# Kernel tuning notes

Hardware: AMD Instinct MI355X
Metric: run time of the kernel (lower is better)

The kernel has to match this reference:

```python
import jax, jax.numpy as jnp
import numpy as np
import math

B, N, D = 4, 1024, 1024
H = 16
HD = D // H          # 64
TOP_K = 64
NUM_STATIC = 32


def setup_inputs() -> dict:
    key = jax.random.key(0)
    ks = jax.random.split(key, 10)
    s = 1.0 / math.sqrt(D)  # ~ nn.Linear default init scale
    inp = {
        "x": jax.random.normal(ks[0], (B, N, D), dtype=jnp.float32),
        "Wq": jax.random.uniform(ks[1], (D, D), jnp.float32, -s, s),
        "bq": jax.random.uniform(ks[2], (D,), jnp.float32, -s, s),
        "Wk": jax.random.uniform(ks[3], (D, D), jnp.float32, -s, s),
        "bk": jax.random.uniform(ks[4], (D,), jnp.float32, -s, s),
        "Wv": jax.random.uniform(ks[5], (D, D), jnp.float32, -s, s),
        "bv": jax.random.uniform(ks[6], (D,), jnp.float32, -s, s),
        "Wo": jax.random.uniform(ks[7], (D, D), jnp.float32, -s, s),
        "bo": jax.random.uniform(ks[8], (D,), jnp.float32, -s, s),
        "static_keys": jax.random.normal(ks[9], (NUM_STATIC, D), dtype=jnp.float32),
    }
    return inp


def _heads(t):
    # [B, N, D] -> [B, H, N, HD]
    return t.reshape(B, N, H, HD).transpose(0, 2, 1, 3)


def reference(x, Wq, bq, Wk, bk, Wv, bv, Wo, bo, static_keys):
    Q = _heads(x @ Wq.T + bq)
    K = _heads(x @ Wk.T + bk)
    V = _heads(x @ Wv.T + bv)

    # Replace the first NUM_STATIC key slots with learned static keys.
    K_stat = static_keys.reshape(1, NUM_STATIC, H, HD).transpose(0, 2, 1, 3)  # [1,H,S,HD]
    K_stat = jnp.broadcast_to(K_stat, (B, H, NUM_STATIC, HD))
    K = jnp.concatenate([K_stat, K[:, :, NUM_STATIC:, :]], axis=2)  # [B,H,N,HD]

    scores = jnp.einsum("bhnd,bhmd->bhnm", Q, K) / math.sqrt(HD)  # [B,H,N,N]

    # top-k mask: keep top_k scores per query, -inf elsewhere
    top_scores, top_idx = jax.lax.top_k(scores, TOP_K)  # [B,H,N,K]
    bi = jnp.arange(B)[:, None, None, None]
    hi = jnp.arange(H)[None, :, None, None]
    ni = jnp.arange(N)[None, None, :, None]
    masked = jnp.full(scores.shape, -jnp.inf, dtype=scores.dtype)
    masked = masked.at[bi, hi, ni, top_idx].set(top_scores)

    attn = jax.nn.softmax(masked, axis=-1)
    out = jnp.einsum("bhnm,bhmd->bhnd", attn, V)  # [B,H,N,HD]
    out = out.transpose(0, 2, 1, 3).reshape(B, N, D)
    return out @ Wo.T + bo
```

## Files before the change

kernel.cpp:

```cpp
#include <hip/hip_runtime.h>

#define NSTAT 32
#define MAXSEL 76

typedef __attribute__((ext_vector_type(8))) short bf16x8_t;
typedef __attribute__((ext_vector_type(4))) float f32x4_t;

#define GLOAD_LDS16(g, l) \
    __builtin_amdgcn_global_load_lds((const __attribute__((address_space(1))) void*)(g), \
                                     (__attribute__((address_space(3))) void*)(l), 16, 0, 0)

__device__ __forceinline__ ushort rtn_bf16(float a) {
    unsigned u = __float_as_uint(a);
    return (ushort)((u + 0x7FFFu + ((u >> 16) & 1u)) >> 16);
}
__device__ __forceinline__ void limb2(float a, ushort& h, ushort& l) {
    ushort hh = rtn_bf16(a);
    float fh = __uint_as_float(((unsigned)hh) << 16);
    float r1 = a - fh;
    l = rtn_bf16(r1);
    h = hh;
}

__global__ __launch_bounds__(256)
void decomp_w_kernel(const float* __restrict__ Wq, const float* __restrict__ Wk,
                     const float* __restrict__ Wv, const float* __restrict__ Wo,
                     ushort* __restrict__ WLq, ushort* __restrict__ WoLb)
{
    const int m = blockIdx.y;
    const float* src = (m == 0) ? Wq : (m == 1) ? Wk : (m == 2) ? Wv : Wo;
    const int idx = blockIdx.x * 256 + threadIdx.x;
    const int e8 = idx * 8;
    const int row = e8 >> 10, k0 = e8 & 1023;
    const int kt = k0 >> 5, q = (k0 >> 3) & 3;
    const size_t doff = ((size_t)row << 10) + (size_t)(kt * 32) + (size_t)((q ^ (row & 3)) * 8);

    float4 v0 = *(const float4*)(src + e8);
    float4 v1 = *(const float4*)(src + e8 + 4);
    float f[8] = {v0.x, v0.y, v0.z, v0.w, v1.x, v1.y, v1.z, v1.w};

    const size_t Mi = (size_t)1 << 20;
    ushort h[8], l[8];
    #pragma unroll
    for (int e = 0; e < 8; ++e) limb2(f[e], h[e], l[e]);
    ushort* H = (m == 3) ? WoLb : WLq + (size_t)(m * 2) * Mi;
    ushort* L = H + Mi;
    *(ushort4*)(H + doff)     = make_ushort4(h[0],h[1],h[2],h[3]);
    *(ushort4*)(H + doff + 4) = make_ushort4(h[4],h[5],h[6],h[7]);
    *(ushort4*)(L + doff)     = make_ushort4(l[0],l[1],l[2],l[3]);
    *(ushort4*)(L + doff + 4) = make_ushort4(l[4],l[5],l[6],l[7]);
}

__global__ __launch_bounds__(256, 3)
void limb_gemm_kernel(const float* __restrict__ A,
                      const ushort* __restrict__ WLq, const ushort* __restrict__ WoLb,
                      const float* __restrict__ bq, const float* __restrict__ bk,
                      const float* __restrict__ bv, const float* __restrict__ bo,
                      const float* __restrict__ statk,
                      float* __restrict__ Qw, float* __restrict__ Vw,
                      ushort* __restrict__ KHo, ushort* __restrict__ KLo,
                      float* __restrict__ Cout, int is_out)
{
    __shared__ __align__(16) ushort Al[2][128][32];
    __shared__ __align__(16) ushort Bl[2][2][128][32];

    const int t = threadIdx.x;
    const int bx = blockIdx.x, by = blockIdx.y;
    const int mode = is_out ? 3 : (int)blockIdx.z;
    const int wc0 = bx * 128;
    const int arow0 = by * 128;

    const size_t Mi = (size_t)1 << 20;
    const ushort* BpH;
    const float* bias;
    if (mode == 0)      { BpH = WLq;          bias = bq; }
    else if (mode == 1) { BpH = WLq + 2*Mi;   bias = bk; }
    else if (mode == 2) { BpH = WLq + 4*Mi;   bias = bv; }
    else                { BpH = WoLb;         bias = bo; }
    const ushort* BpL = BpH + Mi;

    const int ll = t & 63, w = t >> 6;

    f32x4_t acc[4][4];
    #pragma unroll
    for (int i = 0; i < 4; ++i)
        #pragma unroll
        for (int j = 0; j < 4; ++j) acc[i][j] = (f32x4_t){0.f, 0.f, 0.f, 0.f};

    auto stageB = [&](int kt, int bb) {
        #pragma unroll
        for (int limb = 0; limb < 2; ++limb) {
            const ushort* src = limb ? BpL : BpH;
            #pragma unroll
            for (int call = 0; call < 2; ++call) {
                int chunk = (w * 2 + call) * 64 + ll;
                int eoff = chunk * 8;
                int row = eoff >> 5, qp = (eoff >> 3) & 3;
                const ushort* g = src + ((size_t)(wc0 + row) << 10) + kt * 32 + qp * 8;
                char* l = ((char*)&Bl[bb][limb][0][0]) + (w * 2 + call) * 1024;
                GLOAD_LDS16(g, l);
            }
        }
    };
    const int srow = t >> 1, skh = (t & 1) * 16;
    auto loadA = [&](int kt, float4* a4) {
        const float* p = A + (((size_t)(arow0 + srow)) << 10) + kt * 32 + skh;
        a4[0] = *(const float4*)(p + 0);
        a4[1] = *(const float4*)(p + 4);
        a4[2] = *(const float4*)(p + 8);
        a4[3] = *(const float4*)(p + 12);
    };
    auto writeA = [&](const float4* a4) {
        float f[16];
        #pragma unroll
        for (int i = 0; i < 4; ++i) {
            f[i*4+0] = a4[i].x; f[i*4+1] = a4[i].y; f[i*4+2] = a4[i].z; f[i*4+3] = a4[i].w;
        }
        ushort h[16], lo[16];
        #pragma unroll
        for (int e = 0; e < 16; ++e) limb2(f[e], h[e], lo[e]);
        const int sw = srow & 3;
        #pragma unroll
        for (int qq = 0; qq < 2; ++qq) {
            int q = (skh >> 3) + qq;
            int qo = (q ^ sw) * 8;
            bf16x8_t vH, vL;
            #pragma unroll
            for (int e = 0; e < 8; ++e) {
                vH[e] = (short)h[qq*8+e]; vL[e] = (short)lo[qq*8+e];
            }
            *(bf16x8_t*)&Al[0][srow][qo] = vH;
            *(bf16x8_t*)&Al[1][srow][qo] = vL;
        }
    };

    const int wr = (w >> 1) * 64, wcv = (w & 1) * 64;
    const int fr = ll & 15, kg = ll >> 4;

    auto compute = [&](int bb) {
        bf16x8_t af[4][2];
        #pragma unroll
        for (int i = 0; i < 4; ++i) {
            int row = wr + i * 16 + fr;
            int qo = (kg ^ (row & 3)) * 8;
            af[i][0] = *(const bf16x8_t*)&Al[0][row][qo];
            af[i][1] = *(const bf16x8_t*)&Al[1][row][qo];
        }
        #pragma unroll
        for (int j = 0; j < 4; ++j) {
            int row = wcv + j * 16 + fr;
            int qo = (kg ^ (row & 3)) * 8;
            bf16x8_t b0 = *(const bf16x8_t*)&Bl[bb][0][row][qo];
            bf16x8_t b1 = *(const bf16x8_t*)&Bl[bb][1][row][qo];
            #pragma unroll
            for (int i = 0; i < 4; ++i) {
                acc[i][j] = __builtin_amdgcn_mfma_f32_16x16x32_bf16(af[i][0], b0, acc[i][j], 0, 0, 0);
                acc[i][j] = __builtin_amdgcn_mfma_f32_16x16x32_bf16(af[i][0], b1, acc[i][j], 0, 0, 0);
                acc[i][j] = __builtin_amdgcn_mfma_f32_16x16x32_bf16(af[i][1], b0, acc[i][j], 0, 0, 0);
            }
        }
    };

    float4 a4[4];
    loadA(0, a4);
    writeA(a4);
    stageB(0, 0);
    __syncthreads();

    float4 a4n[4];
    for (int kt = 0; kt < 32; ++kt) {
        int bb = kt & 1;
        if (kt < 31) {
            stageB(kt + 1, bb ^ 1);
            loadA(kt + 1, a4n);
        }
        compute(bb);
        __syncthreads();
        if (kt < 31) writeA(a4n);
        __syncthreads();
    }

    #pragma unroll
    for (int i = 0; i < 4; ++i) {
        #pragma unroll
        for (int j = 0; j < 4; ++j) {
            int c = wc0 + wcv + j * 16 + (ll & 15);
            float bv_ = bias[c];
            #pragma unroll
            for (int q = 0; q < 4; ++q) {
                int gr = arow0 + wr + i * 16 + (kg) * 4 + q;
                float v = acc[i][j][q] + bv_;
                if (mode == 3) {
                    Cout[(size_t)gr * 1024 + c] = v;
                } else {
                    int b = gr >> 10, n = gr & 1023;
                    int h = c >> 6, d = c & 63;
                    size_t bhn = ((size_t)(b * 16 + h)) * 1024 + n;
                    if (mode == 1) {
                        if (n < NSTAT) v = statk[n * 1024 + c];
                        ushort kh, klo;
                        limb2(v, kh, klo);
                        size_t off = bhn * 64 + (size_t)(((d >> 3) ^ (n & 7)) * 8) + (d & 7);
                        KHo[off] = kh;
                        KLo[off] = klo;
                    } else {
                        float* Out = (mode == 0) ? Qw : Vw;
                        Out[bhn * 64 + d] = v;
                    }
                }
            }
        }
    }
}

__device__ __forceinline__ void radix_stage7(int* __restrict__ hist, int r, int l,
                                             const unsigned* __restrict__ ku,
                                             unsigned pref, unsigned mask, int shift,
                                             int tgt, int2* __restrict__ piv)
{
    #pragma unroll
    for (int b = 0; b < 8; ++b) hist[(l*8 + b)*33 + r] = 0;
    __syncthreads();
    #pragma unroll
    for (int j = 0; j < 64; ++j) {
        unsigned k = ku[j];
        if ((k & mask) == pref)
            atomicAdd(&hist[(int)((k >> shift) & 127u)*33 + r], 1);
    }
    __syncthreads();
    int seg = 0;
    #pragma unroll
    for (int b = 0; b < 8; ++b) seg += hist[(l*8 + b)*33 + r];
    int suf = seg;
    #pragma unroll
    for (int off = 1; off < 16; off <<= 1) {
        int v = __shfl_down(suf, off, 16);
        suf += (l + off < 16) ? v : 0;
    }
    const int above = suf - seg;
    if (above < tgt && above + seg >= tgt) {
        int c = above;
        #pragma unroll
        for (int b = 7; b >= 0; --b) {
            int h = hist[(l*8 + b)*33 + r];
            if (c + h >= tgt) { piv[r] = make_int2(l*8 + b, tgt - c); break; }
            c += h;
        }
    }
    __syncthreads();
}

__global__ __launch_bounds__(512, 4)
void attn_mfma_kernel(const float* __restrict__ Qw,
                      const ushort* __restrict__ KH, const ushort* __restrict__ KL,
                      const float* __restrict__ Vw, float* __restrict__ outp)
{
    __shared__ __align__(16) char pool[58368];
    __shared__ int2 piv[32];
    __shared__ int defc[32], bndc[32];
    __shared__ float rs_def[32], rs_bnd[32], rowsum[32];

    ushort* Klds0 = (ushort*)pool;
    ushort* Klds1 = Klds0 + 8192;
    int* hist = (int*)pool;
    float (*Qs)[68]  = (float(*)[68])(pool + 32768);
    float (*sc)[132] = (float(*)[132])(pool + 41472);
    uint2 (*sel)[MAXSEL] = (uint2(*)[MAXSEL])(pool + 32768);

    const int t = threadIdx.x;
    const int bid0 = blockIdx.x;
    const int bid = (bid0 & 7) * 256 + (bid0 >> 3);
    const int qt = bid & 31;
    const int bh = bid >> 5;
    const int n0 = qt * 32;
    const float* Qbase = Qw + ((size_t)bh * 1024 + n0) * 64;
    const float* Vbase = Vw + (size_t)bh * 1024 * 64;
    const ushort* KHb = KH + (size_t)bh * 1024 * 64;
    const ushort* KLb = KL + (size_t)bh * 1024 * 64;

    const int ll = t & 63;
    const int w  = t >> 6;
    const int qh = w >> 2;
    const int kr = w & 3;
    const int r  = t >> 4, l = t & 15;

    {
        int q = t >> 4, dq = (t & 15) * 4;
        *(float4*)&Qs[q][dq] = *(const float4*)(Qbase + q * 64 + dq);
    }
    auto stageK = [&](int c) {
        const size_t cb = (size_t)c * 8192;
        #pragma unroll
        for (int i = 0; i < 2; ++i) {
            int boff = i * 8192 + w * 1024;
            GLOAD_LDS16(KHb + cb + boff / 2 + ll * 8, ((char*)Klds0) + boff);
            GLOAD_LDS16(KLb + cb + boff / 2 + ll * 8, ((char*)Klds1) + boff);
        }
    };
    stageK(0);
    __syncthreads();

    bf16x8_t aH[2], aL[2];
    {
        const int arow = qh * 16 + (ll & 15), akg = ll >> 4;
        #pragma unroll
        for (int s = 0; s < 2; ++s) {
            const float* qp = &Qs[arow][s*32 + akg*8];
            float4 q0 = *(const float4*)qp;
            float4 q1 = *(const float4*)(qp + 4);
            float qv[8] = {q0.x,q0.y,q0.z,q0.w,q1.x,q1.y,q1.z,q1.w};
            #pragma unroll
            for (int j = 0; j < 8; ++j) {
                ushort hh, lo2;
                limb2(qv[j], hh, lo2);
                aH[s][j] = (short)hh; aL[s][j] = (short)lo2;
            }
        }
    }
    __syncthreads();

    unsigned ku[64];
    unsigned kumax = 0u;

    #pragma unroll
    for (int c = 0; c < 8; ++c) {
        #pragma unroll
        for (int tile = 0; tile < 2; ++tile) {
            const int m0 = kr * 32 + tile * 16;
            const int brow = m0 + (ll & 15);
            f32x4_t a_ = {0.f, 0.f, 0.f, 0.f};
            #pragma unroll
            for (int s = 0; s < 2; ++s) {
                int q2 = (s*4 + (ll >> 4)) ^ (brow & 7);
                int off = brow*64 + q2*8;
                bf16x8_t bH = *(const bf16x8_t*)&Klds0[off];
                bf16x8_t bL = *(const bf16x8_t*)&Klds1[off];
                a_ = __builtin_amdgcn_mfma_f32_16x16x32_bf16(aH[s], bH, a_, 0, 0, 0);
                a_ = __builtin_amdgcn_mfma_f32_16x16x32_bf16(aH[s], bL, a_, 0, 0, 0);
                a_ = __builtin_amdgcn_mfma_f32_16x16x32_bf16(aL[s], bH, a_, 0, 0, 0);
            }
            const int qr = qh * 16 + (ll >> 4) * 4;
            const int mcol = m0 + (ll & 15);
            sc[qr+0][mcol] = a_[0];
            sc[qr+1][mcol] = a_[1];
            sc[qr+2][mcol] = a_[2];
            sc[qr+3][mcol] = a_[3];
        }
        __syncthreads();

        if (c < 7) stageK(c + 1);
        {
            float4 v0 = *(const float4*)&sc[r][l*8];
            float4 v1 = *(const float4*)&sc[r][l*8 + 4];
            float vv[8] = {v0.x,v0.y,v0.z,v0.w,v1.x,v1.y,v1.z,v1.w};
            #pragma unroll
            for (int e = 0; e < 8; ++e) {
                float vc = fminf(fmaxf(vv[e], -31.9f), 31.9f);
                unsigned q = (unsigned)(int)fmaf(vc, 32768.f, 1048576.f);
                ku[c*8 + e] = q;
                kumax = (q > kumax) ? q : kumax;
            }
        }
        __syncthreads();
    }

    #pragma unroll
    for (int off = 8; off; off >>= 1) {
        unsigned o = __shfl_xor(kumax, off, 16);
        kumax = (o > kumax) ? o : kumax;
    }

    if (t < 32) { defc[t] = 0; bndc[t] = 0; }

    int tgt = 64;
    radix_stage7(hist, r, l, ku, 0u, 0u, 14, tgt, piv);
    unsigned pref = (unsigned)piv[r].x << 14; tgt = piv[r].y;
    radix_stage7(hist, r, l, ku, pref, 0x1FC000u, 7, tgt, piv);
    pref |= (unsigned)piv[r].x << 7; tgt = piv[r].y;
    radix_stage7(hist, r, l, ku, pref, 0x1FFF80u, 0, tgt, piv);
    const unsigned thr = pref | (unsigned)piv[r].x;

    const unsigned bhi = thr + 2u;
    const unsigned blo = thr - 2u;
    float lsd = 0.f, lsb = 0.f;
    #pragma unroll
    for (int j = 0; j < 64; ++j) {
        unsigned k = ku[j];
        if (k > bhi) {
            float wgt = __expf((float)(int)(k - kumax) * 3.814697265625e-6f);
            int slot = atomicAdd(&defc[r], 1);
            sel[r][slot] = make_uint2((unsigned)((j >> 3)*128 + l*8 + (j & 7)), __float_as_uint(wgt));
            lsd += wgt;
        } else if (k >= blo) {
            int bp = atomicAdd(&bndc[r], 1);
            int slot = (MAXSEL - 1) - bp;
            if (slot >= 64) {
                float wgt = __expf((float)(int)(k - kumax) * 3.814697265625e-6f);
                sel[r][slot] = make_uint2((unsigned)((j >> 3)*128 + l*8 + (j & 7)), __float_as_uint(wgt));
                lsb += wgt;
            }
        }
    }
    #pragma unroll
    for (int off = 8; off; off >>= 1) {
        lsd += __shfl_xor(lsd, off, 16);
        lsb += __shfl_xor(lsb, off, 16);
    }
    if (l == 0) { rs_def[r] = lsd; rs_bnd[r] = lsb; }
    __syncthreads();

    if (t < 32) {
        int D = defc[t], m = bndc[t];
        float frac = (float)(64 - D) / (float)m;
        int mm = (m < MAXSEL - 64) ? m : (MAXSEL - 64);
        for (int i = 0; i < mm; ++i) {
            uint2 p = sel[t][(MAXSEL - 1) - i];
            p.y = __float_as_uint(__uint_as_float(p.y) * frac);
            sel[t][(MAXSEL - 1) - i] = p;
        }
        bndc[t] = mm;
        rowsum[t] = rs_def[t] + frac * rs_bnd[t];
    }
    __syncthreads();

    {
        const int pr = t >> 4;
        const int d4 = (t & 15) * 4;
        const int bb = bh >> 4, hh = bh & 15;
        const int D = defc[pr], m = bndc[pr];
        float4 a = make_float4(0.f, 0.f, 0.f, 0.f);
        for (int j = 0; j < D; ++j) {
            uint2 p = sel[pr][j];
            float wv = __uint_as_float(p.y);
            float4 v = *(const float4*)(Vbase + (size_t)p.x * 64 + d4);
            a.x += wv * v.x; a.y += wv * v.y; a.z += wv * v.z; a.w += wv * v.w;
        }
        for (int i = 0; i < m; ++i) {
            uint2 p = sel[pr][(MAXSEL - 1) - i];
            float wv = __uint_as_float(p.y);
            float4 v = *(const float4*)(Vbase + (size_t)p.x * 64 + d4);
            a.x += wv * v.x; a.y += wv * v.y; a.z += wv * v.z; a.w += wv * v.w;
        }
        float inv = 1.0f / rowsum[pr];
        a.x *= inv; a.y *= inv; a.z *= inv; a.w *= inv;
        *(float4*)(outp + ((size_t)bb * 1024 + (n0 + pr)) * 1024 + hh * 64 + d4) = a;
    }
}

extern "C" void kernel_launch(void* const* d_in, const int* in_sizes, int n_in,
                              void* d_out, int out_size, void* d_ws, size_t ws_size,
                              hipStream_t stream) {
    const float* x     = (const float*)d_in[0];
    const float* Wq    = (const float*)d_in[1];
    const float* bq    = (const float*)d_in[2];
    const float* Wk    = (const float*)d_in[3];
    const float* bk    = (const float*)d_in[4];
    const float* Wv    = (const float*)d_in[5];
    const float* bv    = (const float*)d_in[6];
    const float* Wo    = (const float*)d_in[7];
    const float* bo    = (const float*)d_in[8];
    const float* statk = (const float*)d_in[9];
    float* out = (float*)d_out;
    char* base = (char*)d_ws;

    const size_t MiB = (size_t)1 << 20;
    float*  Qw   = (float*)(base);
    float*  Vw   = (float*)(base + 16*MiB);
    ushort* KH   = (ushort*)(base + 32*MiB);
    ushort* KL   = (ushort*)(base + 40*MiB);
    ushort* WoLb = (ushort*)(base + 48*MiB);
    ushort* WLq  = (ushort*)(base + 52*MiB);
    float*  op   = (float*)(base + 52*MiB);

    dim3 gd(512, 4);
    decomp_w_kernel<<<gd, 256, 0, stream>>>(Wq, Wk, Wv, Wo, WLq, WoLb);

    dim3 g1(8, 32, 3);
    limb_gemm_kernel<<<g1, 256, 0, stream>>>(x, WLq, WoLb, bq, bk, bv, bo, statk,
                                             Qw, Vw, KH, KL, nullptr, 0);

    attn_mfma_kernel<<<2048, 512, 0, stream>>>(Qw, KH, KL, Vw, op);

    dim3 g2(8, 32, 1);
    limb_gemm_kernel<<<g2, 256, 0, stream>>>(op, WLq, WoLb, bq, bk, bv, bo, statk,
                                             Qw, Vw, KH, KL, out, 1);
}
```

Before: 302.5 us.

## Double-buffer K tiles with 16 smaller chunks and simplify top-k selection pass

The score loop now processes 16 chunks of 64 keys instead of 8 chunks of 128. K staging for the next chunk goes into a second LDS buffer before the current chunk's MFMA, and scores also alternate between two buffers, so one barrier per iteration is removed and the load overlaps compute. The selection pass collects every candidate at or above the lower bound in one atomic-append list. Exponentials are then computed relative to the threshold instead of a tracked maximum, which drops the max reduction and the serial single-thread boundary rescale. The V gather is unrolled by two to raise memory-level parallelism. Risks are larger LDS use (possibly lower occupancy), a loop that is no longer unrolled, and overflow of the exp if scores sit far above the threshold.

```diff
diff --git a/kernel.cpp b/kernel.cpp
--- a/kernel.cpp
+++ b/kernel.cpp
@@ -255,17 +255,14 @@
                       const ushort* __restrict__ KH, const ushort* __restrict__ KL,
                       const float* __restrict__ Vw, float* __restrict__ outp)
 {
-    __shared__ __align__(16) char pool[58368];
+    __shared__ __align__(16) char pool[59904];
     __shared__ int2 piv[32];
-    __shared__ int defc[32], bndc[32];
-    __shared__ float rs_def[32], rs_bnd[32], rowsum[32];
-
-    ushort* Klds0 = (ushort*)pool;
-    ushort* Klds1 = Klds0 + 8192;
+    __shared__ int cnt[32];
+    __shared__ float rowsum[32];
+
     int* hist = (int*)pool;
-    float (*Qs)[68]  = (float(*)[68])(pool + 32768);
-    float (*sc)[132] = (float(*)[132])(pool + 41472);
-    uint2 (*sel)[MAXSEL] = (uint2(*)[MAXSEL])(pool + 32768);
+    float (*Qs)[68] = (float(*)[68])(pool + 32768);
+    uint2 (*sel)[MAXSEL] = (uint2(*)[MAXSEL])pool;
 
     const int t = threadIdx.x;
     const int bid0 = blockIdx.x;
@@ -288,16 +285,16 @@
         int q = t >> 4, dq = (t & 15) * 4;
         *(float4*)&Qs[q][dq] = *(const float4*)(Qbase + q * 64 + dq);
     }
-    auto stageK = [&](int c) {
-        const size_t cb = (size_t)c * 8192;
-        #pragma unroll
-        for (int i = 0; i < 2; ++i) {
-            int boff = i * 8192 + w * 1024;
-            GLOAD_LDS16(KHb + cb + boff / 2 + ll * 8, ((char*)Klds0) + boff);
-            GLOAD_LDS16(KLb + cb + boff / 2 + ll * 8, ((char*)Klds1) + boff);
-        }
+    auto stageK = [&](int c, int kb) {
+        const ushort* gH = KHb + (size_t)c * 4096 + t * 8;
+        const ushort* gL = KLb + (size_t)c * 4096 + t * 8;
+        char* dH = pool + kb * 16384 + t * 16;
+        char* dL = pool + kb * 16384 + 8192 + t * 16;
+        GLOAD_LDS16(gH, dH);
+        GLOAD_LDS16(gL, dL);
     };
-    stageK(0);
+    stageK(0, 0);
+    if (t < 32) cnt[t] = 0;
     __syncthreads();
 
     bf16x8_t aH[2], aL[2];
@@ -317,60 +314,48 @@
             }
         }
     }
-    __syncthreads();
 
     unsigned ku[64];
-    unsigned kumax = 0u;
-
-    #pragma unroll
-    for (int c = 0; c < 8; ++c) {
-        #pragma unroll
-        for (int tile = 0; tile < 2; ++tile) {
-            const int m0 = kr * 32 + tile * 16;
-            const int brow = m0 + (ll & 15);
+
+    #pragma unroll 1
+    for (int c = 0; c < 16; ++c) {
+        const int kb = c & 1;
+        float (*scb)[72] = (float(*)[72])(pool + 41472 + kb * 9216);
+        if (c < 15) stageK(c + 1, kb ^ 1);
+
+        {
+            const ushort* KH_l = (const ushort*)(pool + kb * 16384);
+            const ushort* KL_l = KH_l + 4096;
+            const int brow = kr * 16 + (ll & 15);
             f32x4_t a_ = {0.f, 0.f, 0.f, 0.f};
             #pragma unroll
             for (int s = 0; s < 2; ++s) {
                 int q2 = (s*4 + (ll >> 4)) ^ (brow & 7);
                 int off = brow*64 + q2*8;
-                bf16x8_t bH = *(const bf16x8_t*)&Klds0[off];
-                bf16x8_t bL = *(const bf16x8_t*)&Klds1[off];
+                bf16x8_t bH = *(const bf16x8_t*)&KH_l[off];
+                bf16x8_t bL = *(const bf16x8_t*)&KL_l[off];
                 a_ = __builtin_amdgcn_mfma_f32_16x16x32_bf16(aH[s], bH, a_, 0, 0, 0);
                 a_ = __builtin_amdgcn_mfma_f32_16x16x32_bf16(aH[s], bL, a_, 0, 0, 0);
                 a_ = __builtin_amdgcn_mfma_f32_16x16x32_bf16(aL[s], bH, a_, 0, 0, 0);
             }
             const int qr = qh * 16 + (ll >> 4) * 4;
-            const int mcol = m0 + (ll & 15);
-            sc[qr+0][mcol] = a_[0];
-            sc[qr+1][mcol] = a_[1];
-            sc[qr+2][mcol] = a_[2];
-            sc[qr+3][mcol] = a_[3];
+            scb[qr+0][brow] = a_[0];
+            scb[qr+1][brow] = a_[1];
+            scb[qr+2][brow] = a_[2];
+            scb[qr+3][brow] = a_[3];
         }
         __syncthreads();
 
-        if (c < 7) stageK(c + 1);
         {
-            float4 v0 = *(const float4*)&sc[r][l*8];
-            float4 v1 = *(const float4*)&sc[r][l*8 + 4];
-            float vv[8] = {v0.x,v0.y,v0.z,v0.w,v1.x,v1.y,v1.z,v1.w};
-            #pragma unroll
-            for (int e = 0; e < 8; ++e) {
+            float4 v4 = *(const float4*)&scb[r][l*4];
+            float vv[4] = {v4.x, v4.y, v4.z, v4.w};
+            #pragma unroll
+            for (int e = 0; e < 4; ++e) {
                 float vc = fminf(fmaxf(vv[e], -31.9f), 31.9f);
-                unsigned q = (unsigned)(int)fmaf(vc, 32768.f, 1048576.f);
-                ku[c*8 + e] = q;
-                kumax = (q > kumax) ? q : kumax;
-            }
-        }
-        __syncthreads();
-    }
-
-    #pragma unroll
-    for (int off = 8; off; off >>= 1) {
-        unsigned o = __shfl_xor(kumax, off, 16);
-        kumax = (o > kumax) ? o : kumax;
-    }
-
-    if (t < 32) { defc[t] = 0; bndc[t] = 0; }
+                ku[c*4 + e] = (unsigned)(int)fmaf(vc, 32768.f, 1048576.f);
+            }
+        }
+    }
 
     int tgt = 64;
     radix_stage7(hist, r, l, ku, 0u, 0u, 14, tgt, piv);
@@ -382,44 +367,42 @@
 
     const unsigned bhi = thr + 2u;
     const unsigned blo = thr - 2u;
-    float lsd = 0.f, lsb = 0.f;
     #pragma unroll
     for (int j = 0; j < 64; ++j) {
         unsigned k = ku[j];
-        if (k > bhi) {
-            float wgt = __expf((float)(int)(k - kumax) * 3.814697265625e-6f);
-            int slot = atomicAdd(&defc[r], 1);
-            sel[r][slot] = make_uint2((unsigned)((j >> 3)*128 + l*8 + (j & 7)), __float_as_uint(wgt));
-            lsd += wgt;
-        } else if (k >= blo) {
-            int bp = atomicAdd(&bndc[r], 1);
-            int slot = (MAXSEL - 1) - bp;
-            if (slot >= 64) {
-                float wgt = __expf((float)(int)(k - kumax) * 3.814697265625e-6f);
-                sel[r][slot] = make_uint2((unsigned)((j >> 3)*128 + l*8 + (j & 7)), __float_as_uint(wgt));
-                lsb += wgt;
-            }
-        }
-    }
-    #pragma unroll
-    for (int off = 8; off; off >>= 1) {
-        lsd += __shfl_xor(lsd, off, 16);
-        lsb += __shfl_xor(lsb, off, 16);
-    }
-    if (l == 0) { rs_def[r] = lsd; rs_bnd[r] = lsb; }
-    __syncthreads();
-
-    if (t < 32) {
-        int D = defc[t], m = bndc[t];
-        float frac = (float)(64 - D) / (float)m;
-        int mm = (m < MAXSEL - 64) ? m : (MAXSEL - 64);
-        for (int i = 0; i < mm; ++i) {
-            uint2 p = sel[t][(MAXSEL - 1) - i];
-            p.y = __float_as_uint(__uint_as_float(p.y) * frac);
-            sel[t][(MAXSEL - 1) - i] = p;
-        }
-        bndc[t] = mm;
-        rowsum[t] = rs_def[t] + frac * rs_bnd[t];
+        if (k >= blo) {
+            int slot = atomicAdd(&cnt[r], 1);
+            if (slot < MAXSEL)
+                sel[r][slot] = make_uint2((unsigned)((j >> 2)*64 + l*4 + (j & 3)), k);
+        }
+    }
+    __syncthreads();
+
+    {
+        int cc = cnt[r]; cc = (cc < MAXSEL) ? cc : MAXSEL;
+        int Dl = 0, ml = 0;
+        for (int j = l; j < cc; j += 16) {
+            unsigned k = sel[r][j].y;
+            if (k > bhi) Dl++; else ml++;
+        }
+        #pragma unroll
+        for (int off = 8; off; off >>= 1) {
+            Dl += __shfl_xor(Dl, off, 16);
+            ml += __shfl_xor(ml, off, 16);
+        }
+        const float frac = (float)(64 - Dl) / (float)ml;
+        float ls = 0.f;
+        for (int j = l; j < cc; j += 16) {
+            uint2 p = sel[r][j];
+            float wgt = __expf((float)(int)(p.y - thr) * 3.814697265625e-6f);
+            if (p.y <= bhi) wgt *= frac;
+            p.y = __float_as_uint(wgt);
+            sel[r][j] = p;
+            ls += wgt;
+        }
+        #pragma unroll
+        for (int off = 8; off; off >>= 1) ls += __shfl_xor(ls, off, 16);
+        if (l == 0) { rowsum[r] = ls; cnt[r] = cc; }
     }
     __syncthreads();
 
@@ -427,16 +410,23 @@
         const int pr = t >> 4;
         const int d4 = (t & 15) * 4;
         const int bb = bh >> 4, hh = bh & 15;
-        const int D = defc[pr], m = bndc[pr];
+        const int cc = cnt[pr];
         float4 a = make_float4(0.f, 0.f, 0.f, 0.f);
-        for (int j = 0; j < D; ++j) {
+        int j = 0;
+        for (; j + 1 < cc; j += 2) {
+            uint2 p0 = sel[pr][j];
+            uint2 p1 = sel[pr][j+1];
+            float w0 = __uint_as_float(p0.y);
+            float w1 = __uint_as_float(p1.y);
+            float4 v0 = *(const float4*)(Vbase + (size_t)p0.x * 64 + d4);
+            float4 v1 = *(const float4*)(Vbase + (size_t)p1.x * 64 + d4);
+            a.x += w0 * v0.x + w1 * v1.x;
+            a.y += w0 * v0.y + w1 * v1.y;
+            a.z += w0 * v0.z + w1 * v1.z;
+            a.w += w0 * v0.w + w1 * v1.w;
+        }
+        if (j < cc) {
             uint2 p = sel[pr][j];
-            float wv = __uint_as_float(p.y);
-            float4 v = *(const float4*)(Vbase + (size_t)p.x * 64 + d4);
-            a.x += wv * v.x; a.y += wv * v.y; a.z += wv * v.z; a.w += wv * v.w;
-        }
-        for (int i = 0; i < m; ++i) {
-            uint2 p = sel[pr][(MAXSEL - 1) - i];
             float wv = __uint_as_float(p.y);
             float4 v = *(const float4*)(Vbase + (size_t)p.x * 64 + d4);
             a.x += wv * v.x; a.y += wv * v.y; a.z += wv * v.z; a.w += wv * v.w;
```

Result: slower. 537.9 us (+77.8%).
